# Kernel tuning notes

Hardware: AMD Instinct MI355X
Metric: run time of the kernel (lower is better)

Reference implementation:

```python
import jax, jax.numpy as jnp
import numpy as np

N_NODES = 50000
N_EDGES = 400000
D_IN = 512
D_OUT = 512
MASK_RATE = 0.3


def setup_inputs() -> dict:
    key = jax.random.key(0)
    k1, k2, k3, k4, k5 = jax.random.split(key, 5)
    feat = jax.random.normal(k1, (N_NODES, D_IN), dtype=jnp.float32)
    # xavier_uniform for weight [in_feat, out_feat]
    limit = float(np.sqrt(6.0 / (D_IN + D_OUT)))
    weight = jax.random.uniform(k2, (D_IN, D_OUT), dtype=jnp.float32, minval=-limit, maxval=limit)
    edge_src = jax.random.randint(k3, (N_EDGES,), 0, N_NODES, dtype=jnp.int64 if jax.config.jax_enable_x64 else jnp.int32)
    edge_dst = jax.random.randint(k4, (N_EDGES,), 0, N_NODES, dtype=jnp.int64 if jax.config.jax_enable_x64 else jnp.int32)
    edge_val = jax.random.uniform(k5, (N_EDGES,), dtype=jnp.float32)
    # deterministic stand-in for torch.randperm(...)[:num_mask]
    perm = jax.random.permutation(jax.random.fold_in(key, 7), N_NODES)
    mask_idx = perm[: int(MASK_RATE * N_NODES)]
    return {
        "feat": feat,
        "weight": weight,
        "edge_val": edge_val,
        "edge_src": edge_src,
        "edge_dst": edge_dst,
        "mask_idx": mask_idx,
    }


def reference(feat, weight, edge_val, edge_src, edge_dst, mask_idx):
    # zero out masked node rows (encoding_mask_noise)
    out_x = feat.at[mask_idx].set(0.0)
    # dense transform: [N, D_in] @ [D_in, D_out]
    x = out_x @ weight
    # spmm(adj, x): for edge (src -> dst, val): out[dst] += val * x[src]
    msgs = edge_val[:, None] * x[edge_src]  # [E, D_out]
    out = jax.ops.segment_sum(msgs, edge_dst, num_segments=feat.shape[0])
    return out, mask_idx
```

## Files before the change

### kernel.cpp

```cpp
#include <hip/hip_runtime.h>

#define DD 512
#define SCAN_B 256
#define BM 128
#define BN 256
#define BK 32
#define NSTEP 16
typedef unsigned short u16;
typedef unsigned int u32;

typedef __attribute__((ext_vector_type(8))) __bf16 bf16v8;
typedef __attribute__((ext_vector_type(4))) float f32x4;

__device__ __forceinline__ u16 f2bf(float f) {
  u32 u = __builtin_bit_cast(u32, f);
  u32 r = (u + 0x7fffu + ((u >> 16) & 1u)) >> 16;
  return (u16)r;
}
__device__ __forceinline__ float bf2f(u32 h) {
  return __builtin_bit_cast(float, h << 16);
}
__device__ __forceinline__ u32 pk2(float a, float b) {
  return f2bf(a) | ((u32)f2bf(b) << 16);
}

typedef const __attribute__((address_space(1))) void* gptr_t;
typedef __attribute__((address_space(3))) void* lptr_t;
__device__ __forceinline__ void gload_lds16(const void* g, void* l) {
  __builtin_amdgcn_global_load_lds((gptr_t)g, (lptr_t)l, 16, 0, 0);
}

#define BAR_N(N)                                                        \
  do {                                                                  \
    __builtin_amdgcn_sched_barrier(0);                                  \
    asm volatile("s_waitcnt vmcnt(" #N ") lgkmcnt(0)\n\ts_barrier" ::: "memory"); \
  } while (0)

__global__ __launch_bounds__(256) void wconv_t(const float* __restrict__ W,
                                               u16* __restrict__ Wt) {
  __shared__ float sm[64][65];
  const int bx = blockIdx.x;
  const int by = blockIdx.y;
  const int t = threadIdx.x;
  const int r = t >> 6;
  const int c = t & 63;
#pragma unroll
  for (int i = 0; i < 64; i += 4)
    sm[i + r][c] = W[(size_t)(bx * 64 + i + r) * DD + by * 64 + c];
  __syncthreads();
#pragma unroll
  for (int i = 0; i < 64; i += 4) {
    const int n = by * 64 + i + r;
    const int k = bx * 64 + c;
    Wt[(size_t)n * DD + k] = f2bf(sm[c][i + r]);
  }
}

__global__ __launch_bounds__(512) void gemm_pipe(const float* __restrict__ A,
                                                 const u16* __restrict__ Bt,
                                                 u16* __restrict__ X, int M) {
  __shared__ __align__(16) u16 ldsA[2][BM * BK];
  __shared__ __align__(16) u16 ldsB[3][BN * BK];
  const int tid = threadIdx.x;
  const int lane = tid & 63;
  const int w = tid >> 6;
  const int wm = w >> 2;
  const int wn = w & 3;
  const int row0 = blockIdx.y * BM;
  const int colB = blockIdx.x * BN;
  const int lr = lane & 15;
  const int kg = lane >> 4;

  f32x4 acc[4][4] = {};

  const int arow = tid >> 2;
  const int agk = (tid & 3) ^ ((arow >> 1) & 3);
  int ar = row0 + arow;
  if (ar >= M) ar = M - 1;
  const float* gA = A + (size_t)ar * DD + agk * 8;
  const int laoff = tid * 8;

  const u16* gB[2];
  int lB[2];
#pragma unroll
  for (int q = 0; q < 2; ++q) {
    const int c = (w * 2 + q) * 64 + lane;
    const int col = c >> 2, kc = c & 3;
    const int gk = kc ^ ((col >> 1) & 3);
    gB[q] = Bt + (size_t)(colB + col) * DD + gk * 8;
    lB[q] = c * 8;
  }

  f32x4 rP[2][2];

#pragma unroll
  for (int q = 0; q < 2; ++q) gload_lds16(gB[q], &ldsB[0][lB[q]]);
#pragma unroll
  for (int q = 0; q < 2; ++q) gload_lds16(gB[q] + BK, &ldsB[1][lB[q]]);
  rP[0][0] = *(const f32x4*)(gA);
  rP[0][1] = *(const f32x4*)(gA + 4);
  rP[1][0] = *(const f32x4*)(gA + BK);
  rP[1][1] = *(const f32x4*)(gA + BK + 4);
  {
    uint4 pk;
    pk.x = pk2(rP[0][0].x, rP[0][0].y);
    pk.y = pk2(rP[0][0].z, rP[0][0].w);
    pk.z = pk2(rP[0][1].x, rP[0][1].y);
    pk.w = pk2(rP[0][1].z, rP[0][1].w);
    *(uint4*)&ldsA[0][laoff] = pk;
  }
  BAR_N(2);

#pragma unroll
  for (int t = 0; t < NSTEP; ++t) {
    if (t + 2 < NSTEP) {
#pragma unroll
      for (int q = 0; q < 2; ++q)
        gload_lds16(gB[q] + (t + 2) * BK, &ldsB[(t + 2) % 3][lB[q]]);
    }

    bf16v8 af[4], bfr[4];
#pragma unroll
    for (int m = 0; m < 4; ++m) {
      const int row = wm * 64 + m * 16 + lr;
      const int kc = kg ^ ((row >> 1) & 3);
      af[m] = *(const bf16v8*)&ldsA[t & 1][row * BK + kc * 8];
    }
#pragma unroll
    for (int n = 0; n < 4; ++n) {
      const int col = wn * 64 + n * 16 + lr;
      const int kc = kg ^ ((col >> 1) & 3);
      bfr[n] = *(const bf16v8*)&ldsB[t % 3][col * BK + kc * 8];
    }
#pragma unroll
    for (int m = 0; m < 4; ++m)
#pragma unroll
      for (int n = 0; n < 4; ++n)
        acc[m][n] = __builtin_amdgcn_mfma_f32_16x16x32_bf16(af[m], bfr[n], acc[m][n], 0, 0, 0);

    if (t + 1 < NSTEP) {
      uint4 pk;
      pk.x = pk2(rP[(t + 1) & 1][0].x, rP[(t + 1) & 1][0].y);
      pk.y = pk2(rP[(t + 1) & 1][0].z, rP[(t + 1) & 1][0].w);
      pk.z = pk2(rP[(t + 1) & 1][1].x, rP[(t + 1) & 1][1].y);
      pk.w = pk2(rP[(t + 1) & 1][1].z, rP[(t + 1) & 1][1].w);
      *(uint4*)&ldsA[(t + 1) & 1][laoff] = pk;
    }
    if (t + 2 < NSTEP) {
      rP[t & 1][0] = *(const f32x4*)(gA + (t + 2) * BK);
      rP[t & 1][1] = *(const f32x4*)(gA + (t + 2) * BK + 4);
    }

    if (t < NSTEP - 3)      BAR_N(4);
    else if (t < NSTEP - 1) BAR_N(0);
  }

  const int crow = (lane >> 4) * 4;
  const int ccol = lane & 15;
#pragma unroll
  for (int m = 0; m < 4; ++m) {
    const int rowb = row0 + wm * 64 + m * 16 + crow;
#pragma unroll
    for (int n = 0; n < 4; ++n) {
      const int col = colB + wn * 64 + n * 16 + ccol;
#pragma unroll
      for (int r = 0; r < 4; ++r)
        X[(size_t)(rowb + r) * DD + col] = f2bf(acc[m][n][r]);
    }
  }
}

__global__ void zero_mask(u16* __restrict__ x, const int* __restrict__ mask,
                          float* __restrict__ out_tail) {
  const int b = blockIdx.x;
  const int r = mask[b];
  if (threadIdx.x == 0) out_tail[b] = (float)r;
  *(uint4*)(x + (size_t)r * DD + threadIdx.x * 8) = make_uint4(0, 0, 0, 0);
}

__global__ __launch_bounds__(256) void hist(const int* __restrict__ dst,
                                            int* __restrict__ counts, int n) {
  const int i = blockIdx.x * blockDim.x + threadIdx.x;
  if (i < n) atomicAdd(&counts[dst[i]], 1);
}

__global__ __launch_bounds__(SCAN_B) void scanA(const int* __restrict__ counts,
                                                int* __restrict__ lscan,
                                                int* __restrict__ blockSums, int n) {
  __shared__ int sm[SCAN_B];
  const int t = threadIdx.x;
  const int i = blockIdx.x * SCAN_B + t;
  const int v = (i < n) ? counts[i] : 0;
  sm[t] = v;
  __syncthreads();
  for (int off = 1; off < SCAN_B; off <<= 1) {
    int add = (t >= off) ? sm[t - off] : 0;
    __syncthreads();
    sm[t] += add;
    __syncthreads();
  }
  if (i < n) lscan[i] = sm[t] - v;
  if (t == SCAN_B - 1) blockSums[blockIdx.x] = sm[t];
}

__global__ __launch_bounds__(SCAN_B) void scanC(int* __restrict__ lscan,
                                                const int* __restrict__ blockSums,
                                                int* __restrict__ cursor, int n, int nb) {
  __shared__ int sm[SCAN_B];
  const int t = threadIdx.x;
  const int v = (t < nb) ? blockSums[t] : 0;
  sm[t] = v;
  __syncthreads();
  for (int off = 1; off < SCAN_B; off <<= 1) {
    int add = (t >= off) ? sm[t - off] : 0;
    __syncthreads();
    sm[t] += add;
    __syncthreads();
  }
  const int base = sm[blockIdx.x] - ((blockIdx.x < nb) ? blockSums[blockIdx.x] : 0);
  const int i = blockIdx.x * SCAN_B + t;
  if (i < n) {
    const int o = lscan[i] + base;
    lscan[i] = o;
    cursor[i] = o;
  }
}

__global__ __launch_bounds__(256) void scatter_sort(const int* __restrict__ src,
                                                    const int* __restrict__ dst,
                                                    const float* __restrict__ ev,
                                                    int* __restrict__ cursor,
                                                    int* __restrict__ ssrc,
                                                    float* __restrict__ sval, int n) {
  const int i = blockIdx.x * blockDim.x + threadIdx.x;
  if (i < n) {
    const int pos = atomicAdd(&cursor[dst[i]], 1);
    ssrc[pos] = src[i];
    sval[pos] = ev[i];
  }
}

__global__ __launch_bounds__(256) void aggregate(const u16* __restrict__ x,
                                                 const int* __restrict__ ssrc,
                                                 const float* __restrict__ sval,
                                                 const int* __restrict__ offsets,
                                                 const int* __restrict__ counts,
                                                 float* __restrict__ out, int n_nodes) {
  const int node = blockIdx.x * 4 + (threadIdx.x >> 6);
  if (node >= n_nodes) return;
  const int lane = threadIdx.x & 63;
  const int b = offsets[node];
  const int e = b + counts[node];
  float acc[8] = {};
  int j = b;
#define AGG1(U, V)                                      \
  do {                                                  \
    acc[0] = fmaf(V, bf2f(U.x & 0xffffu), acc[0]);      \
    acc[1] = fmaf(V, bf2f(U.x >> 16),     acc[1]);      \
    acc[2] = fmaf(V, bf2f(U.y & 0xffffu), acc[2]);      \
    acc[3] = fmaf(V, bf2f(U.y >> 16),     acc[3]);      \
    acc[4] = fmaf(V, bf2f(U.z & 0xffffu), acc[4]);      \
    acc[5] = fmaf(V, bf2f(U.z >> 16),     acc[5]);      \
    acc[6] = fmaf(V, bf2f(U.w & 0xffffu), acc[6]);      \
    acc[7] = fmaf(V, bf2f(U.w >> 16),     acc[7]);      \
  } while (0)
  for (; j + 4 <= e; j += 4) {
    const int s0 = ssrc[j], s1 = ssrc[j + 1], s2 = ssrc[j + 2], s3 = ssrc[j + 3];
    const float v0 = sval[j], v1 = sval[j + 1], v2 = sval[j + 2], v3 = sval[j + 3];
    const uint4 u0 = *(const uint4*)(x + (size_t)s0 * DD + lane * 8);
    const uint4 u1 = *(const uint4*)(x + (size_t)s1 * DD + lane * 8);
    const uint4 u2 = *(const uint4*)(x + (size_t)s2 * DD + lane * 8);
    const uint4 u3 = *(const uint4*)(x + (size_t)s3 * DD + lane * 8);
    AGG1(u0, v0); AGG1(u1, v1); AGG1(u2, v2); AGG1(u3, v3);
  }
  for (; j < e; ++j) {
    const int s = ssrc[j];
    const float v = sval[j];
    const uint4 u = *(const uint4*)(x + (size_t)s * DD + lane * 8);
    AGG1(u, v);
  }
#undef AGG1
  f32x4* o = (f32x4*)(out + (size_t)node * DD + lane * 8);
  f32x4 o0 = {acc[0], acc[1], acc[2], acc[3]};
  f32x4 o1 = {acc[4], acc[5], acc[6], acc[7]};
  __builtin_nontemporal_store(o0, o);
  __builtin_nontemporal_store(o1, o + 1);
}

extern "C" void kernel_launch(void* const* d_in, const int* in_sizes, int n_in,
                              void* d_out, int out_size, void* d_ws, size_t ws_size,
                              hipStream_t stream) {
  const float* feat     = (const float*)d_in[0];
  const float* weight   = (const float*)d_in[1];
  const float* edge_val = (const float*)d_in[2];
  const int*   edge_src = (const int*)d_in[3];
  const int*   edge_dst = (const int*)d_in[4];
  const int*   mask_idx = (const int*)d_in[5];

  const int n_nodes = in_sizes[0] / DD;
  const int n_edges = in_sizes[2];
  const int n_mask  = in_sizes[5];

  const int n_tiles_m = (n_nodes + BM - 1) / BM;
  const int m_pad = n_tiles_m * BM;

  float* out = (float*)d_out;

  char* base = (char*)d_ws;
  size_t off = 0;
  auto alloc = [&](size_t bytes) {
    void* p = base + off;
    off = (off + bytes + 255) & ~(size_t)255;
    return p;
  };
  u16*   x      = (u16*)alloc((size_t)m_pad * DD * sizeof(u16));
  u16*   wt     = (u16*)alloc((size_t)DD * DD * sizeof(u16));
  int*   counts = (int*)alloc((size_t)n_nodes * sizeof(int));
  int*   offs   = (int*)alloc((size_t)n_nodes * sizeof(int));
  int*   cursor = (int*)alloc((size_t)n_nodes * sizeof(int));
  int*   bsums  = (int*)alloc(SCAN_B * sizeof(int));
  int*   ssrc   = (int*)alloc((size_t)n_edges * sizeof(int));
  float* sval   = (float*)alloc((size_t)n_edges * sizeof(float));

  const int nb = (n_nodes + SCAN_B - 1) / SCAN_B;

  (void)hipMemsetAsync(counts, 0, (size_t)n_nodes * sizeof(int), stream);
  hist<<<(n_edges + 255) / 256, 256, 0, stream>>>(edge_dst, counts, n_edges);
  scanA<<<nb, SCAN_B, 0, stream>>>(counts, offs, bsums, n_nodes);
  scanC<<<nb, SCAN_B, 0, stream>>>(offs, bsums, cursor, n_nodes, nb);
  scatter_sort<<<(n_edges + 255) / 256, 256, 0, stream>>>(edge_src, edge_dst, edge_val,
                                                          cursor, ssrc, sval, n_edges);

  dim3 wg(DD / 64, DD / 64);
  wconv_t<<<wg, 256, 0, stream>>>(weight, wt);
  dim3 grid(DD / BN, n_tiles_m);
  gemm_pipe<<<grid, 512, 0, stream>>>(feat, wt, x, n_nodes);
  zero_mask<<<n_mask, 64, 0, stream>>>(x, mask_idx, out + (size_t)n_nodes * DD);

  aggregate<<<(n_nodes + 3) / 4, 256, 0, stream>>>(x, ssrc, sval, offs, counts, out, n_nodes);
}
```

Baseline: 187.9 us.

## Fuse mask zeroing into GEMM A-load via row flags, narrow GEMM N-tile

Builds a per-row byte flag array from mask_idx and applies it as a bitmask when packing A rows to bf16 in the GEMM. This removes the separate zero_mask kernel that rewrote masked rows of X after the GEMM. The GEMM column tile also shrinks from 256 to 128, so each block loads one B chunk per thread and holds a 4x2 accumulator tile per wave. That doubles the block count and lowers register pressure, at the cost of reloading each A tile twice as often. It adds a memset and a small flag kernel.

```diff
diff --git a/kernel.cpp b/kernel.cpp
--- a/kernel.cpp
+++ b/kernel.cpp
@@ -3,11 +3,12 @@
 #define DD 512
 #define SCAN_B 256
 #define BM 128
-#define BN 256
+#define BN 128
 #define BK 32
 #define NSTEP 16
 typedef unsigned short u16;
 typedef unsigned int u32;
+typedef unsigned char u8;
 
 typedef __attribute__((ext_vector_type(8))) __bf16 bf16v8;
 typedef __attribute__((ext_vector_type(4))) float f32x4;
@@ -58,7 +59,8 @@
 
 __global__ __launch_bounds__(512) void gemm_pipe(const float* __restrict__ A,
                                                  const u16* __restrict__ Bt,
-                                                 u16* __restrict__ X, int M) {
+                                                 u16* __restrict__ X,
+                                                 const u8* __restrict__ flg, int M) {
   __shared__ __align__(16) u16 ldsA[2][BM * BK];
   __shared__ __align__(16) u16 ldsB[3][BN * BK];
   const int tid = threadIdx.x;
@@ -71,7 +73,7 @@
   const int lr = lane & 15;
   const int kg = lane >> 4;
 
-  f32x4 acc[4][4] = {};
+  f32x4 acc[4][2] = {};
 
   const int arow = tid >> 2;
   const int agk = (tid & 3) ^ ((arow >> 1) & 3);
@@ -79,47 +81,37 @@
   if (ar >= M) ar = M - 1;
   const float* gA = A + (size_t)ar * DD + agk * 8;
   const int laoff = tid * 8;
-
-  const u16* gB[2];
-  int lB[2];
-#pragma unroll
-  for (int q = 0; q < 2; ++q) {
-    const int c = (w * 2 + q) * 64 + lane;
-    const int col = c >> 2, kc = c & 3;
-    const int gk = kc ^ ((col >> 1) & 3);
-    gB[q] = Bt + (size_t)(colB + col) * DD + gk * 8;
-    lB[q] = c * 8;
-  }
+  const u32 akeep = flg[ar] ? 0u : 0xFFFFFFFFu;
+
+  const int bcol = tid >> 2;
+  const int bgk = (tid & 3) ^ ((bcol >> 1) & 3);
+  const u16* gB = Bt + (size_t)(colB + bcol) * DD + bgk * 8;
+  const int lboff = tid * 8;
 
   f32x4 rP[2][2];
 
-#pragma unroll
-  for (int q = 0; q < 2; ++q) gload_lds16(gB[q], &ldsB[0][lB[q]]);
-#pragma unroll
-  for (int q = 0; q < 2; ++q) gload_lds16(gB[q] + BK, &ldsB[1][lB[q]]);
+  gload_lds16(gB, &ldsB[0][lboff]);
+  gload_lds16(gB + BK, &ldsB[1][lboff]);
   rP[0][0] = *(const f32x4*)(gA);
   rP[0][1] = *(const f32x4*)(gA + 4);
   rP[1][0] = *(const f32x4*)(gA + BK);
   rP[1][1] = *(const f32x4*)(gA + BK + 4);
   {
     uint4 pk;
-    pk.x = pk2(rP[0][0].x, rP[0][0].y);
-    pk.y = pk2(rP[0][0].z, rP[0][0].w);
-    pk.z = pk2(rP[0][1].x, rP[0][1].y);
-    pk.w = pk2(rP[0][1].z, rP[0][1].w);
+    pk.x = pk2(rP[0][0].x, rP[0][0].y) & akeep;
+    pk.y = pk2(rP[0][0].z, rP[0][0].w) & akeep;
+    pk.z = pk2(rP[0][1].x, rP[0][1].y) & akeep;
+    pk.w = pk2(rP[0][1].z, rP[0][1].w) & akeep;
     *(uint4*)&ldsA[0][laoff] = pk;
   }
   BAR_N(2);
 
 #pragma unroll
   for (int t = 0; t < NSTEP; ++t) {
-    if (t + 2 < NSTEP) {
-#pragma unroll
-      for (int q = 0; q < 2; ++q)
-        gload_lds16(gB[q] + (t + 2) * BK, &ldsB[(t + 2) % 3][lB[q]]);
-    }
-
-    bf16v8 af[4], bfr[4];
+    if (t + 2 < NSTEP)
+      gload_lds16(gB + (t + 2) * BK, &ldsB[(t + 2) % 3][lboff]);
+
+    bf16v8 af[4], bfr[2];
 #pragma unroll
     for (int m = 0; m < 4; ++m) {
       const int row = wm * 64 + m * 16 + lr;
@@ -127,23 +119,23 @@
       af[m] = *(const bf16v8*)&ldsA[t & 1][row * BK + kc * 8];
     }
 #pragma unroll
-    for (int n = 0; n < 4; ++n) {
-      const int col = wn * 64 + n * 16 + lr;
+    for (int n = 0; n < 2; ++n) {
+      const int col = wn * 32 + n * 16 + lr;
       const int kc = kg ^ ((col >> 1) & 3);
       bfr[n] = *(const bf16v8*)&ldsB[t % 3][col * BK + kc * 8];
     }
 #pragma unroll
     for (int m = 0; m < 4; ++m)
 #pragma unroll
-      for (int n = 0; n < 4; ++n)
+      for (int n = 0; n < 2; ++n)
         acc[m][n] = __builtin_amdgcn_mfma_f32_16x16x32_bf16(af[m], bfr[n], acc[m][n], 0, 0, 0);
 
     if (t + 1 < NSTEP) {
       uint4 pk;
-      pk.x = pk2(rP[(t + 1) & 1][0].x, rP[(t + 1) & 1][0].y);
-      pk.y = pk2(rP[(t + 1) & 1][0].z, rP[(t + 1) & 1][0].w);
-      pk.z = pk2(rP[(t + 1) & 1][1].x, rP[(t + 1) & 1][1].y);
-      pk.w = pk2(rP[(t + 1) & 1][1].z, rP[(t + 1) & 1][1].w);
+      pk.x = pk2(rP[(t + 1) & 1][0].x, rP[(t + 1) & 1][0].y) & akeep;
+      pk.y = pk2(rP[(t + 1) & 1][0].z, rP[(t + 1) & 1][0].w) & akeep;
+      pk.z = pk2(rP[(t + 1) & 1][1].x, rP[(t + 1) & 1][1].y) & akeep;
+      pk.w = pk2(rP[(t + 1) & 1][1].z, rP[(t + 1) & 1][1].w) & akeep;
       *(uint4*)&ldsA[(t + 1) & 1][laoff] = pk;
     }
     if (t + 2 < NSTEP) {
@@ -151,7 +143,7 @@
       rP[t & 1][1] = *(const f32x4*)(gA + (t + 2) * BK + 4);
     }
 
-    if (t < NSTEP - 3)      BAR_N(4);
+    if (t < NSTEP - 3)      BAR_N(3);
     else if (t < NSTEP - 1) BAR_N(0);
   }
 
@@ -161,8 +153,8 @@
   for (int m = 0; m < 4; ++m) {
     const int rowb = row0 + wm * 64 + m * 16 + crow;
 #pragma unroll
-    for (int n = 0; n < 4; ++n) {
-      const int col = colB + wn * 64 + n * 16 + ccol;
+    for (int n = 0; n < 2; ++n) {
+      const int col = colB + wn * 32 + n * 16 + ccol;
 #pragma unroll
       for (int r = 0; r < 4; ++r)
         X[(size_t)(rowb + r) * DD + col] = f2bf(acc[m][n][r]);
@@ -170,12 +162,15 @@
   }
 }
 
-__global__ void zero_mask(u16* __restrict__ x, const int* __restrict__ mask,
-                          float* __restrict__ out_tail) {
-  const int b = blockIdx.x;
-  const int r = mask[b];
-  if (threadIdx.x == 0) out_tail[b] = (float)r;
-  *(uint4*)(x + (size_t)r * DD + threadIdx.x * 8) = make_uint4(0, 0, 0, 0);
+__global__ __launch_bounds__(256) void flag_build(const int* __restrict__ mask,
+                                                  u8* __restrict__ flg,
+                                                  float* __restrict__ out_tail, int nm) {
+  const int i = blockIdx.x * blockDim.x + threadIdx.x;
+  if (i < nm) {
+    const int r = mask[i];
+    flg[r] = 1;
+    out_tail[i] = (float)r;
+  }
 }
 
 __global__ __launch_bounds__(256) void hist(const int* __restrict__ dst,
@@ -321,21 +316,24 @@
   int*   bsums  = (int*)alloc(SCAN_B * sizeof(int));
   int*   ssrc   = (int*)alloc((size_t)n_edges * sizeof(int));
   float* sval   = (float*)alloc((size_t)n_edges * sizeof(float));
+  u8*    flg    = (u8*)alloc((size_t)m_pad);
 
   const int nb = (n_nodes + SCAN_B - 1) / SCAN_B;
 
   (void)hipMemsetAsync(counts, 0, (size_t)n_nodes * sizeof(int), stream);
+  (void)hipMemsetAsync(flg, 0, (size_t)m_pad, stream);
   hist<<<(n_edges + 255) / 256, 256, 0, stream>>>(edge_dst, counts, n_edges);
   scanA<<<nb, SCAN_B, 0, stream>>>(counts, offs, bsums, n_nodes);
   scanC<<<nb, SCAN_B, 0, stream>>>(offs, bsums, cursor, n_nodes, nb);
   scatter_sort<<<(n_edges + 255) / 256, 256, 0, stream>>>(edge_src, edge_dst, edge_val,
                                                           cursor, ssrc, sval, n_edges);
+  flag_build<<<(n_mask + 255) / 256, 256, 0, stream>>>(mask_idx, flg,
+                                                       out + (size_t)n_nodes * DD, n_mask);
 
   dim3 wg(DD / 64, DD / 64);
   wconv_t<<<wg, 256, 0, stream>>>(weight, wt);
   dim3 grid(DD / BN, n_tiles_m);
-  gemm_pipe<<<grid, 512, 0, stream>>>(feat, wt, x, n_nodes);
-  zero_mask<<<n_mask, 64, 0, stream>>>(x, mask_idx, out + (size_t)n_nodes * DD);
+  gemm_pipe<<<grid, 512, 0, stream>>>(feat, wt, x, flg, n_nodes);
 
   aggregate<<<(n_nodes + 3) / 4, 256, 0, stream>>>(x, ssrc, sval, offs, counts, out, n_nodes);
 }
```

New measurement: 207.8 us. 1.11x slower.
